# Optimization experiments

Measured on AMD Instinct MI355X. Metric: run time of the kernel, lower is better.

## Reference

```python
import jax, jax.numpy as jnp
import numpy as np

DN = ('NDHWC', 'DHWIO', 'NDHWC')
EPS = 1e-5  # torch BatchNorm default

def _conv(x, w, s):
    # Minkowski conv, kernel 3 centered: output coord j gathers input coords s*j + {-1,0,1}
    return jax.lax.conv_general_dilated(x, w, (s, s, s), ((1, 1),) * 3, dimension_numbers=DN)

def _convt(x, w):
    # stride-2 transpose conv, kernel 3 centered: output p gets input c where 2c in {p-1,p,p+1}
    return jax.lax.conv_general_dilated(x, w, (1, 1, 1), ((1, 2),) * 3,
                                        lhs_dilation=(2, 2, 2), dimension_numbers=DN)

def _down(m):
    # stride-2 coordinate map: a coarse voxel is active iff any of its 2x2x2 fine voxels is
    B, G = m.shape[0], m.shape[1]
    return m.reshape(B, G // 2, 2, G // 2, 2, G // 2, 2).any(axis=(2, 4, 6))

def _mbn(h, m, g, b):
    # MinkowskiBatchNorm: BatchNorm1d over the active (sparse) feature rows only
    mf = m[..., None].astype(h.dtype)
    h = h * mf
    cnt = jnp.maximum(jnp.sum(mf), 1.0)
    mean = jnp.sum(h, axis=(0, 1, 2, 3)) / cnt
    var = jnp.sum(((h - mean) * mf) ** 2, axis=(0, 1, 2, 3)) / cnt
    return ((h - mean) * jax.lax.rsqrt(var + EPS) * g + b) * mf


def setup_inputs() -> dict:
    key = jax.random.key(0)
    ks = jax.random.split(key, 8)
    B, G, Cin, Cout = 2, 64, 4, 16
    def w(k, shape, fan):
        return jax.random.normal(k, shape, jnp.float32) * np.float32(1.0 / np.sqrt(fan))
    return {
        'x': jax.random.normal(ks[0], (B, G, G, G, Cin), jnp.float32),
        'mask': jax.random.bernoulli(ks[1], 0.1, (B, G, G, G)),
        'w1': w(ks[2], (3, 3, 3, Cin, 8), 27 * Cin), 'g1': jnp.ones(8), 'b1': jnp.zeros(8),
        'w2': w(ks[3], (3, 3, 3, 8, 16), 27 * 8), 'g2': jnp.ones(16), 'b2': jnp.zeros(16),
        'w3': w(ks[4], (3, 3, 3, 16, 32), 27 * 16), 'g3': jnp.ones(32), 'b3': jnp.zeros(32),
        'w3t': w(ks[5], (3, 3, 3, 32, 16), 27 * 32), 'g3t': jnp.ones(16), 'b3t': jnp.zeros(16),
        'w2t': w(ks[6], (3, 3, 3, 32, 16), 27 * 32), 'g2t': jnp.ones(16), 'b2t': jnp.zeros(16),
        'w1x1': w(ks[7], (24, Cout), 24),
    }


def reference(x, mask, w1, g1, b1, w2, g2, b2, w3, g3, b3,
              w3t, g3t, b3t, w2t, g2t, b2t, w1x1):
    m1 = mask
    m2 = _down(m1)
    m4 = _down(m2)
    mf1 = m1[..., None].astype(x.dtype)

    xs = x * mf1                                      # sparse tensor: zero at inactive coords
    s1 = _mbn(_conv(xs, w1, 1), m1, g1, b1)           # block1, stride 1
    o = jax.nn.relu(s1)
    s2 = _mbn(_conv(o, w2, 2), m2, g2, b2)            # block2, stride 2
    o = jax.nn.relu(s2)
    s4 = _mbn(_conv(o, w3, 2), m4, g3, b3)            # block3, stride 4
    o = jax.nn.relu(s4)

    o = jax.nn.relu(_mbn(_convt(o, w3t), m2, g3t, b3t))   # block3_tr -> stride-2 coords
    o = jnp.concatenate([o, s2], axis=-1)                 # ME.cat(out, out_s2) -> 32 ch
    o = jax.nn.relu(_mbn(_convt(o, w2t), m1, g2t, b2t))   # block2_tr -> stride-1 coords
    o = jnp.concatenate([o, s1], axis=-1)                 # ME.cat(out, out_s1) -> 24 ch
    return jnp.einsum('bdhwc,co->bdhwo', o, w1x1) * mf1   # conv1_tr: 1x1x1 conv
```

## Files before the change

### kernel.cpp

```cpp
#include <hip/hip_runtime.h>

#define NVOX1 524288
#define NVOX2 65536
#define NVOX4 8192

#define ST_SUM1 16
#define ST_SQ1  24
#define ST_SUM2 32
#define ST_SQ2  48
#define ST_SUM3 64
#define ST_SQ3  96
#define ST_SUM3T 128
#define ST_SQ3T  144
#define ST_SUM2T 160
#define ST_SQ2T  176
#define FLAG_OFF 200
#define IC_N1 204
#define IC_N2 205
#define IC_N4 206
#define ST_ZERO 256

#define OFF_M1C 512
#define OFF_M2  (OFF_M1C + NVOX1)
#define OFF_M4  (OFF_M2 + NVOX2)
#define OFF_H1  (OFF_M4 + NVOX4)
#define OFF_S2  (OFF_H1 + NVOX1 * 8)
#define OFF_H3  (OFF_S2 + NVOX2 * 16)
#define OFF_T3  (OFF_H3 + NVOX4 * 32)
#define OFF_L1  (OFF_T3 + NVOX2 * 16)
#define OFF_L2  (OFF_L1 + NVOX1)
#define OFF_L4  (OFF_L2 + NVOX2)
#define OFF_BC1 (OFF_L4 + NVOX4)
#define OFF_BC2 (OFF_BC1 + 2048)
#define OFF_BC4 (OFF_BC2 + 256)

#define EPSBN 1e-5f

__device__ __forceinline__ void ttaps(int p, int gin, int* c, int* k, int* ok) {
  c[0] = p >> 1; k[0] = (p & 1) ? 0 : 1; ok[0] = 1;
  int cb = (p + 1) >> 1;
  int o = (p & 1) && (cb < gin);
  c[1] = o ? cb : 0; k[1] = 2; ok[1] = o;
}

__global__ __launch_bounds__(256) void k_detect(const unsigned int* __restrict__ m,
                                                int* __restrict__ flags) {
  int tid = blockIdx.x * 256 + threadIdx.x;
  int hasf = 0, hasb = 0;
  for (int i = tid; i < NVOX1; i += 256 * 256) {
    unsigned int v = m[i];
    if (v == 0x3F800000u) hasf = 1;
    else if (v > 1u) hasb = 1;
  }
  hasf = __syncthreads_or(hasf);
  hasb = __syncthreads_or(hasb);
  if (threadIdx.x == 0) {
    if (hasf) atomicOr(&flags[0], 1);
    if (hasb) atomicOr(&flags[1], 1);
  }
}

__global__ __launch_bounds__(256) void k_canon(const void* __restrict__ mraw,
                                               int* __restrict__ m1c,
                                               const int* __restrict__ flags,
                                               int* __restrict__ blkcnt1) {
  int idx = blockIdx.x * 256 + threadIdx.x;
  int isf = flags[0], isb = flags[1];
  int v;
  if (isf)      v = (((const float*)mraw)[idx] != 0.f);
  else if (isb) v = (((const unsigned char*)mraw)[idx] != 0);
  else          v = (((const int*)mraw)[idx] != 0);
  m1c[idx] = v;
  int c = __syncthreads_count(v);
  if (threadIdx.x == 0) blkcnt1[blockIdx.x] = c;
}

__global__ __launch_bounds__(256) void k_down1(const int* __restrict__ m1,
                                               int* __restrict__ m2,
                                               int* __restrict__ blkcnt2) {
  int idx = blockIdx.x * 256 + threadIdx.x;
  int x = idx & 31, y = (idx >> 5) & 31, z = (idx >> 10) & 31, b = idx >> 15;
  int any = 0;
#pragma unroll
  for (int dz = 0; dz < 2; dz++)
#pragma unroll
    for (int dy = 0; dy < 2; dy++)
#pragma unroll
      for (int dx = 0; dx < 2; dx++)
        any |= m1[((b * 64 + 2 * z + dz) * 64 + 2 * y + dy) * 64 + 2 * x + dx];
  any = any ? 1 : 0;
  m2[idx] = any;
  int c = __syncthreads_count(any);
  if (threadIdx.x == 0) blkcnt2[blockIdx.x] = c;
}

__global__ __launch_bounds__(256) void k_down2(const int* __restrict__ m2,
                                               int* __restrict__ m4,
                                               int* __restrict__ blkcnt4) {
  int idx = blockIdx.x * 256 + threadIdx.x;
  int x = idx & 15, y = (idx >> 4) & 15, z = (idx >> 8) & 15, b = idx >> 12;
  int any = 0;
#pragma unroll
  for (int dz = 0; dz < 2; dz++)
#pragma unroll
    for (int dy = 0; dy < 2; dy++)
#pragma unroll
      for (int dx = 0; dx < 2; dx++)
        any |= m2[((b * 32 + 2 * z + dz) * 32 + 2 * y + dy) * 32 + 2 * x + dx];
  any = any ? 1 : 0;
  m4[idx] = any;
  int c = __syncthreads_count(any);
  if (threadIdx.x == 0) blkcnt4[blockIdx.x] = c;
}

__global__ __launch_bounds__(1024) void k_scan(int* __restrict__ bc1,
                                               int* __restrict__ bc2,
                                               int* __restrict__ bc4,
                                               int* __restrict__ cnts) {
  __shared__ int sA[2048], sB[2048];
  int* a; int n; int outIdx;
  if (blockIdx.x == 0)      { a = bc1; n = 2048; outIdx = IC_N1; }
  else if (blockIdx.x == 1) { a = bc2; n = 256;  outIdx = IC_N2; }
  else                      { a = bc4; n = 32;   outIdx = IC_N4; }
  int t = threadIdx.x;
  int i0 = t, i1 = t + 1024;
  int v0 = (i0 < n) ? a[i0] : 0;
  int v1 = (i1 < n) ? a[i1] : 0;
  sA[i0] = v0; sA[i1] = v1;
  __syncthreads();
  int* src = sA; int* dst = sB;
  for (int st = 1; st < 2048; st <<= 1) {
    int x0 = src[i0]; if (i0 >= st) x0 += src[i0 - st];
    int x1 = src[i1]; if (i1 >= st) x1 += src[i1 - st];
    dst[i0] = x0; dst[i1] = x1;
    __syncthreads();
    int* tmp = src; src = dst; dst = tmp;
  }
  if (i0 < n) a[i0] = src[i0] - v0;
  if (i1 < n) a[i1] = src[i1] - v1;
  if (t == 0) cnts[outIdx] = src[2047];
}

__global__ __launch_bounds__(256) void k_scatter(const int* __restrict__ m1,
                                                 const int* __restrict__ m2,
                                                 const int* __restrict__ m4,
                                                 const int* __restrict__ bc1,
                                                 const int* __restrict__ bc2,
                                                 const int* __restrict__ bc4,
                                                 int* __restrict__ list1,
                                                 int* __restrict__ list2,
                                                 int* __restrict__ list4) {
  __shared__ int s_w[4];
  int bid = blockIdx.x, t = threadIdx.x;
  const int* mask; const int* base; int* list; int lb;
  if (bid < 2048)      { mask = m1; base = bc1; list = list1; lb = bid; }
  else if (bid < 2304) { mask = m2; base = bc2; list = list2; lb = bid - 2048; }
  else                 { mask = m4; base = bc4; list = list4; lb = bid - 2304; }
  int idx = lb * 256 + t;
  int act = mask[idx];
  unsigned long long b = __ballot(act != 0);
  int lane = t & 63, wid = t >> 6;
  if (lane == 0) s_w[wid] = __popcll(b);
  __syncthreads();
  int wbase = 0;
  for (int i = 0; i < wid; i++) wbase += s_w[i];
  if (act) {
    int pre = __popcll(b & ((1ull << lane) - 1ull));
    list[base[lb] + wbase + pre] = idx;
  }
}

__global__ __launch_bounds__(256) void k_conv1(const float* __restrict__ x,
                                               const int* __restrict__ m1,
                                               const int* __restrict__ list1,
                                               const int* __restrict__ cnts,
                                               const float* __restrict__ w,
                                               float* __restrict__ h1,
                                               float* __restrict__ stats) {
  __shared__ float s_w[27 * 32];
  __shared__ float s_sum[8], s_sq[8];
  int t = threadIdx.x;
  { const float4* w4 = (const float4*)w; float4* sw4 = (float4*)s_w;
    for (int i = t; i < 216; i += 256) sw4[i] = w4[i]; }
  if (t < 8) { s_sum[t] = 0.f; s_sq[t] = 0.f; }
  __syncthreads();
  int n = cnts[IC_N1];
  float sum[8], sq[8];
#pragma unroll
  for (int c = 0; c < 8; c++) { sum[c] = 0.f; sq[c] = 0.f; }
  for (int i = blockIdx.x * 256 + t; i < n; i += gridDim.x * 256) {
    int v = list1[i];
    int vx = v & 63, vy = (v >> 6) & 63, vz = (v >> 12) & 63, vb = v >> 18;
    float acc[8];
#pragma unroll
    for (int c = 0; c < 8; c++) acc[c] = 0.f;
#pragma unroll
    for (int kd = 0; kd < 3; kd++) { int d = vz + kd - 1; if ((unsigned)d >= 64u) continue;
#pragma unroll
      for (int kh = 0; kh < 3; kh++) { int h = vy + kh - 1; if ((unsigned)h >= 64u) continue;
#pragma unroll
        for (int kw = 0; kw < 3; kw++) { int ww = vx + kw - 1; if ((unsigned)ww >= 64u) continue;
          int ni = ((vb * 64 + d) * 64 + h) * 64 + ww;
          if (!m1[ni]) continue;
          float4 ip = *(const float4*)(x + (size_t)ni * 4);
          const float* wp = s_w + ((kd * 3 + kh) * 3 + kw) * 32;
#pragma unroll
          for (int co = 0; co < 8; co++) {
            float a = fmaf(ip.x, wp[co], acc[co]);
            a = fmaf(ip.y, wp[8 + co], a);
            a = fmaf(ip.z, wp[16 + co], a);
            acc[co] = fmaf(ip.w, wp[24 + co], a);
          }
        } } }
    float4* hp = (float4*)(h1 + (size_t)v * 8);
    float4 q0 = {acc[0], acc[1], acc[2], acc[3]};
    float4 q1 = {acc[4], acc[5], acc[6], acc[7]};
    hp[0] = q0; hp[1] = q1;
#pragma unroll
    for (int c = 0; c < 8; c++) { sum[c] += acc[c]; sq[c] += acc[c] * acc[c]; }
  }
#pragma unroll
  for (int off = 1; off < 64; off <<= 1)
#pragma unroll
    for (int c = 0; c < 8; c++) {
      sum[c] += __shfl_xor(sum[c], off, 64);
      sq[c]  += __shfl_xor(sq[c], off, 64);
    }
  if ((t & 63) == 0) {
#pragma unroll
    for (int c = 0; c < 8; c++) { atomicAdd(&s_sum[c], sum[c]); atomicAdd(&s_sq[c], sq[c]); }
  }
  __syncthreads();
  if (t < 8) {
    if (s_sum[t] != 0.f) atomicAdd(&stats[ST_SUM1 + t], s_sum[t]);
    if (s_sq[t]  != 0.f) atomicAdd(&stats[ST_SQ1 + t], s_sq[t]);
  }
}

__global__ __launch_bounds__(256) void k_conv2(const float* __restrict__ h1,
                                               const int* __restrict__ m1,
                                               const int* __restrict__ list2,
                                               const int* __restrict__ cnts,
                                               const float* __restrict__ w,
                                               const float* __restrict__ g1,
                                               const float* __restrict__ b1,
                                               float* __restrict__ s2,
                                               float* __restrict__ stats) {
  __shared__ float s_w[27 * 128];
  __shared__ float s_sc[8], s_bi[8];
  __shared__ float s_sum[16], s_sq[16];
  int t = threadIdx.x;
  { const float4* w4 = (const float4*)w; float4* sw4 = (float4*)s_w;
    for (int i = t; i < 864; i += 256) sw4[i] = w4[i]; }
  if (t < 8) {
    float cnt = fmaxf((float)cnts[IC_N1], 1.f);
    float mean = stats[ST_SUM1 + t] / cnt;
    float var = fmaxf(stats[ST_SQ1 + t] / cnt - mean * mean, 0.f);
    float sc = g1[t] * rsqrtf(var + EPSBN);
    s_sc[t] = sc; s_bi[t] = b1[t] - mean * sc;
  }
  if (t < 16) { s_sum[t] = 0.f; s_sq[t] = 0.f; }
  __syncthreads();
  int n = cnts[IC_N2];
  float sum[16], sq[16];
#pragma unroll
  for (int c = 0; c < 16; c++) { sum[c] = 0.f; sq[c] = 0.f; }
  for (int i = blockIdx.x * 256 + t; i < n; i += gridDim.x * 256) {
    int v = list2[i];
    int vx = v & 31, vy = (v >> 5) & 31, vz = (v >> 10) & 31, vb = v >> 15;
    float acc[16];
#pragma unroll
    for (int c = 0; c < 16; c++) acc[c] = 0.f;
#pragma unroll
    for (int kd = 0; kd < 3; kd++) { int d = 2 * vz + kd - 1; if (d < 0) continue;
#pragma unroll
      for (int kh = 0; kh < 3; kh++) { int h = 2 * vy + kh - 1; if (h < 0) continue;
#pragma unroll
        for (int kw = 0; kw < 3; kw++) { int ww = 2 * vx + kw - 1; if (ww < 0) continue;
          int ni = ((vb * 64 + d) * 64 + h) * 64 + ww;
          if (!m1[ni]) continue;
          float4 i0 = *(const float4*)(h1 + (size_t)ni * 8);
          float4 i1 = *(const float4*)(h1 + (size_t)ni * 8 + 4);
          float r[8] = {i0.x, i0.y, i0.z, i0.w, i1.x, i1.y, i1.z, i1.w};
          const float* wp = s_w + ((kd * 3 + kh) * 3 + kw) * 128;
#pragma unroll
          for (int ci = 0; ci < 8; ci++) {
            float vv = fmaxf(fmaf(r[ci], s_sc[ci], s_bi[ci]), 0.f);
#pragma unroll
            for (int co = 0; co < 16; co++) acc[co] = fmaf(vv, wp[ci * 16 + co], acc[co]);
          }
        } } }
    float4* sp = (float4*)(s2 + (size_t)v * 16);
#pragma unroll
    for (int cq = 0; cq < 4; cq++) {
      float4 q = {acc[cq * 4 + 0], acc[cq * 4 + 1], acc[cq * 4 + 2], acc[cq * 4 + 3]};
      sp[cq] = q;
    }
#pragma unroll
    for (int c = 0; c < 16; c++) { sum[c] += acc[c]; sq[c] += acc[c] * acc[c]; }
  }
#pragma unroll
  for (int off = 1; off < 64; off <<= 1)
#pragma unroll
    for (int c = 0; c < 16; c++) {
      sum[c] += __shfl_xor(sum[c], off, 64);
      sq[c]  += __shfl_xor(sq[c], off, 64);
    }
  if ((t & 63) == 0) {
#pragma unroll
    for (int c = 0; c < 16; c++) { atomicAdd(&s_sum[c], sum[c]); atomicAdd(&s_sq[c], sq[c]); }
  }
  __syncthreads();
  if (t < 16) {
    if (s_sum[t] != 0.f) atomicAdd(&stats[ST_SUM2 + t], s_sum[t]);
    if (s_sq[t]  != 0.f) atomicAdd(&stats[ST_SQ2 + t], s_sq[t]);
  }
}

__global__ __launch_bounds__(256) void k_conv3(const float* __restrict__ s2raw,
                                               const int* __restrict__ m2,
                                               const int* __restrict__ list4,
                                               const int* __restrict__ cnts,
                                               const float* __restrict__ w,
                                               const float* __restrict__ g2,
                                               const float* __restrict__ b2,
                                               float* __restrict__ h3,
                                               float* __restrict__ stats) {
  __shared__ float s_w[27 * 512];
  __shared__ float s_sc[16], s_bi[16];
  __shared__ float s_sum[32], s_sq[32];
  int t = threadIdx.x;
  { const float4* w4 = (const float4*)w; float4* sw4 = (float4*)s_w;
    for (int i = t; i < 3456; i += 256) sw4[i] = w4[i]; }
  if (t < 16) {
    float cnt = fmaxf((float)cnts[IC_N2], 1.f);
    float mean = stats[ST_SUM2 + t] / cnt;
    float var = fmaxf(stats[ST_SQ2 + t] / cnt - mean * mean, 0.f);
    float sc = g2[t] * rsqrtf(var + EPSBN);
    s_sc[t] = sc; s_bi[t] = b2[t] - mean * sc;
  }
  if (t < 32) { s_sum[t] = 0.f; s_sq[t] = 0.f; }
  __syncthreads();
  int cog = t & 3;
  int n = cnts[IC_N4] * 4;
  float sum[8], sq[8];
#pragma unroll
  for (int c = 0; c < 8; c++) { sum[c] = 0.f; sq[c] = 0.f; }
  for (int i = blockIdx.x * 256 + t; i < n; i += gridDim.x * 256) {
    int li = i >> 2;
    int v = list4[li];
    int vx = v & 15, vy = (v >> 4) & 15, vz = (v >> 8) & 15, vb = v >> 12;
    float acc[8];
#pragma unroll
    for (int c = 0; c < 8; c++) acc[c] = 0.f;
#pragma unroll
    for (int kd = 0; kd < 3; kd++) { int d = 2 * vz + kd - 1; if (d < 0) continue;
#pragma unroll
      for (int kh = 0; kh < 3; kh++) { int h = 2 * vy + kh - 1; if (h < 0) continue;
#pragma unroll
        for (int kw = 0; kw < 3; kw++) { int ww = 2 * vx + kw - 1; if (ww < 0) continue;
          int ni = ((vb * 32 + d) * 32 + h) * 32 + ww;
          if (!m2[ni]) continue;
          const float4* ip = (const float4*)(s2raw + (size_t)ni * 16);
          const float* wp = s_w + ((kd * 3 + kh) * 3 + kw) * 512 + cog * 8;
#pragma unroll
          for (int cq = 0; cq < 4; cq++) {
            float4 q = ip[cq];
            float rr[4] = {q.x, q.y, q.z, q.w};
#pragma unroll
            for (int j = 0; j < 4; j++) {
              int ci = cq * 4 + j;
              float vv = fmaxf(fmaf(rr[j], s_sc[ci], s_bi[ci]), 0.f);
#pragma unroll
              for (int co = 0; co < 8; co++) acc[co] = fmaf(vv, wp[ci * 32 + co], acc[co]);
            }
          }
        } } }
    float4* hp = (float4*)(h3 + (size_t)v * 32 + cog * 8);
    float4 q0 = {acc[0], acc[1], acc[2], acc[3]};
    float4 q1 = {acc[4], acc[5], acc[6], acc[7]};
    hp[0] = q0; hp[1] = q1;
#pragma unroll
    for (int c = 0; c < 8; c++) { sum[c] += acc[c]; sq[c] += acc[c] * acc[c]; }
  }
#pragma unroll
  for (int off = 4; off < 64; off <<= 1)
#pragma unroll
    for (int c = 0; c < 8; c++) {
      sum[c] += __shfl_xor(sum[c], off, 64);
      sq[c]  += __shfl_xor(sq[c], off, 64);
    }
  if ((t & 63) < 4) {
#pragma unroll
    for (int c = 0; c < 8; c++) {
      atomicAdd(&s_sum[cog * 8 + c], sum[c]);
      atomicAdd(&s_sq[cog * 8 + c], sq[c]);
    }
  }
  __syncthreads();
  if (t < 32) {
    if (s_sum[t] != 0.f) atomicAdd(&stats[ST_SUM3 + t], s_sum[t]);
    if (s_sq[t]  != 0.f) atomicAdd(&stats[ST_SQ3 + t], s_sq[t]);
  }
}

__global__ __launch_bounds__(256) void k_convt3(const float* __restrict__ h3raw,
                                                const int* __restrict__ m4,
                                                const int* __restrict__ list2,
                                                const int* __restrict__ cnts,
                                                const float* __restrict__ w,
                                                const float* __restrict__ g3,
                                                const float* __restrict__ b3,
                                                float* __restrict__ t3,
                                                float* __restrict__ stats) {
  __shared__ float s_w[27 * 512];
  __shared__ float s_sc[32], s_bi[32];
  __shared__ float s_sum[16], s_sq[16];
  int t = threadIdx.x;
  { const float4* w4 = (const float4*)w; float4* sw4 = (float4*)s_w;
    for (int i = t; i < 3456; i += 256) sw4[i] = w4[i]; }
  if (t < 32) {
    float cnt = fmaxf((float)cnts[IC_N4], 1.f);
    float mean = stats[ST_SUM3 + t] / cnt;
    float var = fmaxf(stats[ST_SQ3 + t] / cnt - mean * mean, 0.f);
    float sc = g3[t] * rsqrtf(var + EPSBN);
    s_sc[t] = sc; s_bi[t] = b3[t] - mean * sc;
  }
  if (t < 16) { s_sum[t] = 0.f; s_sq[t] = 0.f; }
  __syncthreads();
  int cog = t & 1;
  int n = cnts[IC_N2] * 2;
  float sum[8], sq[8];
#pragma unroll
  for (int c = 0; c < 8; c++) { sum[c] = 0.f; sq[c] = 0.f; }
  for (int i = blockIdx.x * 256 + t; i < n; i += gridDim.x * 256) {
    int li = i >> 1;
    int v = list2[li];
    int px = v & 31, py = (v >> 5) & 31, pz = (v >> 10) & 31, vb = v >> 15;
    int czv[2], kzv[2], okz[2], cyv[2], kyv[2], oky[2], cxv[2], kxv[2], okx[2];
    ttaps(pz, 16, czv, kzv, okz);
    ttaps(py, 16, cyv, kyv, oky);
    ttaps(px, 16, cxv, kxv, okx);
    float acc[8];
#pragma unroll
    for (int c = 0; c < 8; c++) acc[c] = 0.f;
#pragma unroll
    for (int dz = 0; dz < 2; dz++)
#pragma unroll
      for (int dy = 0; dy < 2; dy++)
#pragma unroll
        for (int dx = 0; dx < 2; dx++) {
          if (!(okz[dz] & oky[dy] & okx[dx])) continue;
          int ni = ((vb * 16 + czv[dz]) * 16 + cyv[dy]) * 16 + cxv[dx];
          if (!m4[ni]) continue;
          const float4* ip = (const float4*)(h3raw + (size_t)ni * 32);
          const float* wp = s_w + ((kzv[dz] * 3 + kyv[dy]) * 3 + kxv[dx]) * 512 + cog * 8;
#pragma unroll
          for (int cq = 0; cq < 8; cq++) {
            float4 q = ip[cq];
            float rr[4] = {q.x, q.y, q.z, q.w};
#pragma unroll
            for (int j = 0; j < 4; j++) {
              int ci = cq * 4 + j;
              float vv = fmaxf(fmaf(rr[j], s_sc[ci], s_bi[ci]), 0.f);
#pragma unroll
              for (int co = 0; co < 8; co++) acc[co] = fmaf(vv, wp[ci * 16 + co], acc[co]);
            }
          }
        }
    float4* op = (float4*)(t3 + (size_t)v * 16 + cog * 8);
    float4 q0 = {acc[0], acc[1], acc[2], acc[3]};
    float4 q1 = {acc[4], acc[5], acc[6], acc[7]};
    op[0] = q0; op[1] = q1;
#pragma unroll
    for (int c = 0; c < 8; c++) { sum[c] += acc[c]; sq[c] += acc[c] * acc[c]; }
  }
#pragma unroll
  for (int off = 2; off < 64; off <<= 1)
#pragma unroll
    for (int c = 0; c < 8; c++) {
      sum[c] += __shfl_xor(sum[c], off, 64);
      sq[c]  += __shfl_xor(sq[c], off, 64);
    }
  if ((t & 63) < 2) {
#pragma unroll
    for (int c = 0; c < 8; c++) {
      atomicAdd(&s_sum[cog * 8 + c], sum[c]);
      atomicAdd(&s_sq[cog * 8 + c], sq[c]);
    }
  }
  __syncthreads();
  if (t < 16) {
    if (s_sum[t] != 0.f) atomicAdd(&stats[ST_SUM3T + t], s_sum[t]);
    if (s_sq[t]  != 0.f) atomicAdd(&stats[ST_SQ3T + t], s_sq[t]);
  }
}

__global__ __launch_bounds__(256) void k_convt2(const float* __restrict__ t3raw,
                                                const float* __restrict__ s2raw,
                                                const int* __restrict__ m2,
                                                const int* __restrict__ list1,
                                                const int* __restrict__ cnts,
                                                const float* __restrict__ w,
                                                const float* __restrict__ g3t,
                                                const float* __restrict__ b3t,
                                                const float* __restrict__ g2,
                                                const float* __restrict__ b2,
                                                float* __restrict__ outraw,
                                                float* __restrict__ stats) {
  __shared__ float s_w[27 * 512];
  __shared__ float s_sct[16], s_bit[16], s_sc2[16], s_bi2[16];
  __shared__ float s_sum[16], s_sq[16];
  int t = threadIdx.x;
  { const float4* w4 = (const float4*)w; float4* sw4 = (float4*)s_w;
    for (int i = t; i < 3456; i += 256) sw4[i] = w4[i]; }
  if (t < 16) {
    float cnt = fmaxf((float)cnts[IC_N2], 1.f);
    float mean = stats[ST_SUM3T + t] / cnt;
    float var = fmaxf(stats[ST_SQ3T + t] / cnt - mean * mean, 0.f);
    float sc = g3t[t] * rsqrtf(var + EPSBN);
    s_sct[t] = sc; s_bit[t] = b3t[t] - mean * sc;
    float mean2 = stats[ST_SUM2 + t] / cnt;
    float var2 = fmaxf(stats[ST_SQ2 + t] / cnt - mean2 * mean2, 0.f);
    float sc2 = g2[t] * rsqrtf(var2 + EPSBN);
    s_sc2[t] = sc2; s_bi2[t] = b2[t] - mean2 * sc2;
    s_sum[t] = 0.f; s_sq[t] = 0.f;
  }
  __syncthreads();
  int cog = t & 1;
  int n = cnts[IC_N1] * 2;
  float sum[8], sq[8];
#pragma unroll
  for (int c = 0; c < 8; c++) { sum[c] = 0.f; sq[c] = 0.f; }
  for (int i = blockIdx.x * 256 + t; i < n; i += gridDim.x * 256) {
    int li = i >> 1;
    int v = list1[li];
    int px = v & 63, py = (v >> 6) & 63, pz = (v >> 12) & 63, vb = v >> 18;
    int czv[2], kzv[2], okz[2], cyv[2], kyv[2], oky[2], cxv[2], kxv[2], okx[2];
    ttaps(pz, 32, czv, kzv, okz);
    ttaps(py, 32, cyv, kyv, oky);
    ttaps(px, 32, cxv, kxv, okx);
    float acc[8];
#pragma unroll
    for (int c = 0; c < 8; c++) acc[c] = 0.f;
#pragma unroll
    for (int dz = 0; dz < 2; dz++)
#pragma unroll
      for (int dy = 0; dy < 2; dy++)
#pragma unroll
        for (int dx = 0; dx < 2; dx++) {
          if (!(okz[dz] & oky[dy] & okx[dx])) continue;
          int ni = ((vb * 32 + czv[dz]) * 32 + cyv[dy]) * 32 + cxv[dx];
          if (!m2[ni]) continue;
          const float4* tp = (const float4*)(t3raw + (size_t)ni * 16);
          const float4* sp = (const float4*)(s2raw + (size_t)ni * 16);
          const float* wp = s_w + ((kzv[dz] * 3 + kyv[dy]) * 3 + kxv[dx]) * 512 + cog * 8;
#pragma unroll
          for (int cq = 0; cq < 4; cq++) {
            float4 q = tp[cq];
            float rr[4] = {q.x, q.y, q.z, q.w};
#pragma unroll
            for (int j = 0; j < 4; j++) {
              int ci = cq * 4 + j;
              float vv = fmaxf(fmaf(rr[j], s_sct[ci], s_bit[ci]), 0.f);
#pragma unroll
              for (int co = 0; co < 8; co++) acc[co] = fmaf(vv, wp[ci * 16 + co], acc[co]);
            }
          }
#pragma unroll
          for (int cq = 0; cq < 4; cq++) {
            float4 q = sp[cq];
            float rr[4] = {q.x, q.y, q.z, q.w};
#pragma unroll
            for (int j = 0; j < 4; j++) {
              int ci = cq * 4 + j;
              float vv = fmaf(rr[j], s_sc2[ci], s_bi2[ci]);
#pragma unroll
              for (int co = 0; co < 8; co++) acc[co] = fmaf(vv, wp[(16 + ci) * 16 + co], acc[co]);
            }
          }
        }
    float4* op = (float4*)(outraw + (size_t)v * 16 + cog * 8);
    float4 q0 = {acc[0], acc[1], acc[2], acc[3]};
    float4 q1 = {acc[4], acc[5], acc[6], acc[7]};
    op[0] = q0; op[1] = q1;
#pragma unroll
    for (int c = 0; c < 8; c++) { sum[c] += acc[c]; sq[c] += acc[c] * acc[c]; }
  }
#pragma unroll
  for (int off = 2; off < 64; off <<= 1)
#pragma unroll
    for (int c = 0; c < 8; c++) {
      sum[c] += __shfl_xor(sum[c], off, 64);
      sq[c]  += __shfl_xor(sq[c], off, 64);
    }
  if ((t & 63) < 2) {
#pragma unroll
    for (int c = 0; c < 8; c++) {
      atomicAdd(&s_sum[cog * 8 + c], sum[c]);
      atomicAdd(&s_sq[cog * 8 + c], sq[c]);
    }
  }
  __syncthreads();
  if (t < 16) {
    if (s_sum[t] != 0.f) atomicAdd(&stats[ST_SUM2T + t], s_sum[t]);
    if (s_sq[t]  != 0.f) atomicAdd(&stats[ST_SQ2T + t], s_sq[t]);
  }
}

__global__ __launch_bounds__(256) void k_final(float* __restrict__ out,
                                               const float* __restrict__ h1raw,
                                               const int* __restrict__ list1,
                                               const int* __restrict__ cnts,
                                               const float* __restrict__ g2t,
                                               const float* __restrict__ b2t,
                                               const float* __restrict__ g1,
                                               const float* __restrict__ b1,
                                               const float* __restrict__ w1x1,
                                               const float* __restrict__ stats) {
  __shared__ float s_sc[16], s_bi[16], s_sc1[8], s_bi1[8], s_w[384];
  int t = threadIdx.x;
  for (int i = t; i < 384; i += 256) s_w[i] = w1x1[i];
  if (t < 16) {
    float cnt = fmaxf((float)cnts[IC_N1], 1.f);
    float mean = stats[ST_SUM2T + t] / cnt;
    float var = fmaxf(stats[ST_SQ2T + t] / cnt - mean * mean, 0.f);
    float sc = g2t[t] * rsqrtf(var + EPSBN);
    s_sc[t] = sc; s_bi[t] = b2t[t] - mean * sc;
  }
  if (t < 8) {
    float cnt = fmaxf((float)cnts[IC_N1], 1.f);
    float mean = stats[ST_SUM1 + t] / cnt;
    float var = fmaxf(stats[ST_SQ1 + t] / cnt - mean * mean, 0.f);
    float sc = g1[t] * rsqrtf(var + EPSBN);
    s_sc1[t] = sc; s_bi1[t] = b1[t] - mean * sc;
  }
  __syncthreads();
  int n = cnts[IC_N1];
  for (int i = blockIdx.x * 256 + t; i < n; i += gridDim.x * 256) {
    int v = list1[i];
    float* op = out + (size_t)v * 16;
    float t2[16];
    {
      const float4* op4 = (const float4*)op;
#pragma unroll
      for (int cq = 0; cq < 4; cq++) {
        float4 q = op4[cq];
        t2[cq * 4 + 0] = fmaxf(fmaf(q.x, s_sc[cq * 4 + 0], s_bi[cq * 4 + 0]), 0.f);
        t2[cq * 4 + 1] = fmaxf(fmaf(q.y, s_sc[cq * 4 + 1], s_bi[cq * 4 + 1]), 0.f);
        t2[cq * 4 + 2] = fmaxf(fmaf(q.z, s_sc[cq * 4 + 2], s_bi[cq * 4 + 2]), 0.f);
        t2[cq * 4 + 3] = fmaxf(fmaf(q.w, s_sc[cq * 4 + 3], s_bi[cq * 4 + 3]), 0.f);
      }
    }
    float s1v[8];
    {
      const float4* sp4 = (const float4*)(h1raw + (size_t)v * 8);
#pragma unroll
      for (int cq = 0; cq < 2; cq++) {
        float4 q = sp4[cq];
        s1v[cq * 4 + 0] = fmaf(q.x, s_sc1[cq * 4 + 0], s_bi1[cq * 4 + 0]);
        s1v[cq * 4 + 1] = fmaf(q.y, s_sc1[cq * 4 + 1], s_bi1[cq * 4 + 1]);
        s1v[cq * 4 + 2] = fmaf(q.z, s_sc1[cq * 4 + 2], s_bi1[cq * 4 + 2]);
        s1v[cq * 4 + 3] = fmaf(q.w, s_sc1[cq * 4 + 3], s_bi1[cq * 4 + 3]);
      }
    }
    float o[16];
#pragma unroll
    for (int oc = 0; oc < 16; oc++) o[oc] = 0.f;
#pragma unroll
    for (int c = 0; c < 16; c++) {
      float vv = t2[c];
#pragma unroll
      for (int oc = 0; oc < 16; oc++) o[oc] = fmaf(vv, s_w[c * 16 + oc], o[oc]);
    }
#pragma unroll
    for (int c = 0; c < 8; c++) {
      float vv = s1v[c];
#pragma unroll
      for (int oc = 0; oc < 16; oc++) o[oc] = fmaf(vv, s_w[(16 + c) * 16 + oc], o[oc]);
    }
    float4* op4 = (float4*)op;
#pragma unroll
    for (int cq = 0; cq < 4; cq++) {
      float4 q = {o[cq * 4 + 0], o[cq * 4 + 1], o[cq * 4 + 2], o[cq * 4 + 3]};
      op4[cq] = q;
    }
  }
}

extern "C" void kernel_launch(void* const* d_in, const int* in_sizes, int n_in,
                              void* d_out, int out_size, void* d_ws, size_t ws_size,
                              hipStream_t stream) {
  const float* x    = (const float*)d_in[0];
  const void*  mraw = d_in[1];
  const float* w1   = (const float*)d_in[2];
  const float* g1   = (const float*)d_in[3];
  const float* b1   = (const float*)d_in[4];
  const float* w2   = (const float*)d_in[5];
  const float* g2   = (const float*)d_in[6];
  const float* b2   = (const float*)d_in[7];
  const float* w3   = (const float*)d_in[8];
  const float* g3   = (const float*)d_in[9];
  const float* b3   = (const float*)d_in[10];
  const float* w3t  = (const float*)d_in[11];
  const float* g3t  = (const float*)d_in[12];
  const float* b3t  = (const float*)d_in[13];
  const float* w2t  = (const float*)d_in[14];
  const float* g2t  = (const float*)d_in[15];
  const float* b2t  = (const float*)d_in[16];
  const float* w1x1 = (const float*)d_in[17];

  float* ws = (float*)d_ws;
  float* stats = ws;
  int* cnts = (int*)ws;
  int* flags = (int*)(ws + FLAG_OFF);
  int* m1c = (int*)(ws + OFF_M1C);
  int* m2  = (int*)(ws + OFF_M2);
  int* m4  = (int*)(ws + OFF_M4);
  float* h1 = ws + OFF_H1;
  float* s2 = ws + OFF_S2;
  float* h3 = ws + OFF_H3;
  float* t3 = ws + OFF_T3;
  int* list1 = (int*)(ws + OFF_L1);
  int* list2 = (int*)(ws + OFF_L2);
  int* list4 = (int*)(ws + OFF_L4);
  int* bc1 = (int*)(ws + OFF_BC1);
  int* bc2 = (int*)(ws + OFF_BC2);
  int* bc4 = (int*)(ws + OFF_BC4);
  float* out = (float*)d_out;

  hipMemsetAsync(ws, 0, ST_ZERO * sizeof(float), stream);
  hipMemsetAsync(d_out, 0, (size_t)out_size * sizeof(float), stream);
  k_detect<<<256, 256, 0, stream>>>((const unsigned int*)mraw, flags);
  k_canon<<<NVOX1 / 256, 256, 0, stream>>>(mraw, m1c, flags, bc1);
  k_down1<<<NVOX2 / 256, 256, 0, stream>>>(m1c, m2, bc2);
  k_down2<<<NVOX4 / 256, 256, 0, stream>>>(m2, m4, bc4);
  k_scan<<<3, 1024, 0, stream>>>(bc1, bc2, bc4, cnts);
  k_scatter<<<2048 + 256 + 32, 256, 0, stream>>>(m1c, m2, m4, bc1, bc2, bc4, list1, list2, list4);
  k_conv1<<<256, 256, 0, stream>>>(x, m1c, list1, cnts, w1, h1, stats);
  k_conv2<<<256, 256, 0, stream>>>(h1, m1c, list2, cnts, w2, g1, b1, s2, stats);
  k_conv3<<<512, 256, 0, stream>>>(s2, m2, list4, cnts, w3, g2, b2, h3, stats);
  k_convt3<<<512, 256, 0, stream>>>(h3, m4, list2, cnts, w3t, g3, b3, t3, stats);
  k_convt2<<<512, 256, 0, stream>>>(t3, s2, m2, list1, cnts, w2t, g3t, b3t, g2, b2, out, stats);
  k_final<<<256, 256, 0, stream>>>(out, h1, list1, cnts, g2t, b2t, g1, b1, w1x1, stats);
}
```

Before: 192.8 us.

## Split output channels across blockIdx.y and stage only per-group weights in LDS

```diff
diff --git a/kernel.cpp b/kernel.cpp
--- a/kernel.cpp
+++ b/kernel.cpp
@@ -41,6 +41,20 @@
   int cb = (p + 1) >> 1;
   int o = (p & 1) && (cb < gin);
   c[1] = o ? cb : 0; k[1] = 2; ok[1] = o;
+}
+
+__device__ __forceinline__ void stat_flush8(float* sum, float* sq, float* s_sum, float* s_sq, int t) {
+#pragma unroll
+  for (int off = 1; off < 64; off <<= 1)
+#pragma unroll
+    for (int c = 0; c < 8; c++) {
+      sum[c] += __shfl_xor(sum[c], off, 64);
+      sq[c]  += __shfl_xor(sq[c], off, 64);
+    }
+  if ((t & 63) == 0) {
+#pragma unroll
+    for (int c = 0; c < 8; c++) { atomicAdd(&s_sum[c], sum[c]); atomicAdd(&s_sq[c], sq[c]); }
+  }
 }
 
 __global__ __launch_bounds__(256) void k_detect(const unsigned int* __restrict__ m,
@@ -219,17 +233,7 @@
 #pragma unroll
     for (int c = 0; c < 8; c++) { sum[c] += acc[c]; sq[c] += acc[c] * acc[c]; }
   }
-#pragma unroll
-  for (int off = 1; off < 64; off <<= 1)
-#pragma unroll
-    for (int c = 0; c < 8; c++) {
-      sum[c] += __shfl_xor(sum[c], off, 64);
-      sq[c]  += __shfl_xor(sq[c], off, 64);
-    }
-  if ((t & 63) == 0) {
-#pragma unroll
-    for (int c = 0; c < 8; c++) { atomicAdd(&s_sum[c], sum[c]); atomicAdd(&s_sq[c], sq[c]); }
-  }
+  stat_flush8(sum, sq, s_sum, s_sq, t);
   __syncthreads();
   if (t < 8) {
     if (s_sum[t] != 0.f) atomicAdd(&stats[ST_SUM1 + t], s_sum[t]);
@@ -246,31 +250,33 @@
                                                const float* __restrict__ b1,
                                                float* __restrict__ s2,
                                                float* __restrict__ stats) {
-  __shared__ float s_w[27 * 128];
+  __shared__ float s_w[27 * 8 * 8];
   __shared__ float s_sc[8], s_bi[8];
-  __shared__ float s_sum[16], s_sq[16];
-  int t = threadIdx.x;
-  { const float4* w4 = (const float4*)w; float4* sw4 = (float4*)s_w;
-    for (int i = t; i < 864; i += 256) sw4[i] = w4[i]; }
+  __shared__ float s_sum[8], s_sq[8];
+  int t = threadIdx.x, g = blockIdx.y;
+  for (int i = t; i < 432; i += 256) {
+    int r = i >> 1, half = i & 1;
+    *(float4*)(s_w + r * 8 + half * 4) = *(const float4*)(w + r * 16 + g * 8 + half * 4);
+  }
   if (t < 8) {
     float cnt = fmaxf((float)cnts[IC_N1], 1.f);
     float mean = stats[ST_SUM1 + t] / cnt;
     float var = fmaxf(stats[ST_SQ1 + t] / cnt - mean * mean, 0.f);
     float sc = g1[t] * rsqrtf(var + EPSBN);
     s_sc[t] = sc; s_bi[t] = b1[t] - mean * sc;
-  }
-  if (t < 16) { s_sum[t] = 0.f; s_sq[t] = 0.f; }
+    s_sum[t] = 0.f; s_sq[t] = 0.f;
+  }
   __syncthreads();
   int n = cnts[IC_N2];
-  float sum[16], sq[16];
-#pragma unroll
-  for (int c = 0; c < 16; c++) { sum[c] = 0.f; sq[c] = 0.f; }
+  float sum[8], sq[8];
+#pragma unroll
+  for (int c = 0; c < 8; c++) { sum[c] = 0.f; sq[c] = 0.f; }
   for (int i = blockIdx.x * 256 + t; i < n; i += gridDim.x * 256) {
     int v = list2[i];
     int vx = v & 31, vy = (v >> 5) & 31, vz = (v >> 10) & 31, vb = v >> 15;
-    float acc[16];
-#pragma unroll
-    for (int c = 0; c < 16; c++) acc[c] = 0.f;
+    float acc[8];
+#pragma unroll
+    for (int c = 0; c < 8; c++) acc[c] = 0.f;
 #pragma unroll
     for (int kd = 0; kd < 3; kd++) { int d = 2 * vz + kd - 1; if (d < 0) continue;
 #pragma unroll
@@ -282,38 +288,26 @@
           float4 i0 = *(const float4*)(h1 + (size_t)ni * 8);
           float4 i1 = *(const float4*)(h1 + (size_t)ni * 8 + 4);
           float r[8] = {i0.x, i0.y, i0.z, i0.w, i1.x, i1.y, i1.z, i1.w};
-          const float* wp = s_w + ((kd * 3 + kh) * 3 + kw) * 128;
+          const float* wp = s_w + ((kd * 3 + kh) * 3 + kw) * 64;
 #pragma unroll
           for (int ci = 0; ci < 8; ci++) {
             float vv = fmaxf(fmaf(r[ci], s_sc[ci], s_bi[ci]), 0.f);
 #pragma unroll
-            for (int co = 0; co < 16; co++) acc[co] = fmaf(vv, wp[ci * 16 + co], acc[co]);
+            for (int co = 0; co < 8; co++) acc[co] = fmaf(vv, wp[ci * 8 + co], acc[co]);
           }
         } } }
-    float4* sp = (float4*)(s2 + (size_t)v * 16);
-#pragma unroll
-    for (int cq = 0; cq < 4; cq++) {
-      float4 q = {acc[cq * 4 + 0], acc[cq * 4 + 1], acc[cq * 4 + 2], acc[cq * 4 + 3]};
-      sp[cq] = q;
-    }
-#pragma unroll
-    for (int c = 0; c < 16; c++) { sum[c] += acc[c]; sq[c] += acc[c] * acc[c]; }
-  }
-#pragma unroll
-  for (int off = 1; off < 64; off <<= 1)
-#pragma unroll
-    for (int c = 0; c < 16; c++) {
-      sum[c] += __shfl_xor(sum[c], off, 64);
-      sq[c]  += __shfl_xor(sq[c], off, 64);
-    }
-  if ((t & 63) == 0) {
-#pragma unroll
-    for (int c = 0; c < 16; c++) { atomicAdd(&s_sum[c], sum[c]); atomicAdd(&s_sq[c], sq[c]); }
-  }
-  __syncthreads();
-  if (t < 16) {
-    if (s_sum[t] != 0.f) atomicAdd(&stats[ST_SUM2 + t], s_sum[t]);
-    if (s_sq[t]  != 0.f) atomicAdd(&stats[ST_SQ2 + t], s_sq[t]);
+    float4* sp = (float4*)(s2 + (size_t)v * 16 + g * 8);
+    float4 q0 = {acc[0], acc[1], acc[2], acc[3]};
+    float4 q1 = {acc[4], acc[5], acc[6], acc[7]};
+    sp[0] = q0; sp[1] = q1;
+#pragma unroll
+    for (int c = 0; c < 8; c++) { sum[c] += acc[c]; sq[c] += acc[c] * acc[c]; }
+  }
+  stat_flush8(sum, sq, s_sum, s_sq, t);
+  __syncthreads();
+  if (t < 8) {
+    if (s_sum[t] != 0.f) atomicAdd(&stats[ST_SUM2 + g * 8 + t], s_sum[t]);
+    if (s_sq[t]  != 0.f) atomicAdd(&stats[ST_SQ2 + g * 8 + t], s_sq[t]);
   }
 }
 
@@ -326,12 +320,14 @@
                                                const float* __restrict__ b2,
                                                float* __restrict__ h3,
                                                float* __restrict__ stats) {
-  __shared__ float s_w[27 * 512];
+  __shared__ float s_w[27 * 16 * 8];
   __shared__ float s_sc[16], s_bi[16];
-  __shared__ float s_sum[32], s_sq[32];
-  int t = threadIdx.x;
-  { const float4* w4 = (const float4*)w; float4* sw4 = (float4*)s_w;
-    for (int i = t; i < 3456; i += 256) sw4[i] = w4[i]; }
+  __shared__ float s_sum[8], s_sq[8];
+  int t = threadIdx.x, g = blockIdx.y;
+  for (int i = t; i < 864; i += 256) {
+    int r = i >> 1, half = i & 1;
+    *(float4*)(s_w + r * 8 + half * 4) = *(const float4*)(w + r * 32 + g * 8 + half * 4);
+  }
   if (t < 16) {
     float cnt = fmaxf((float)cnts[IC_N2], 1.f);
     float mean = stats[ST_SUM2 + t] / cnt;
@@ -339,16 +335,14 @@
     float sc = g2[t] * rsqrtf(var + EPSBN);
     s_sc[t] = sc; s_bi[t] = b2[t] - mean * sc;
   }
-  if (t < 32) { s_sum[t] = 0.f; s_sq[t] = 0.f; }
-  __syncthreads();
-  int cog = t & 3;
-  int n = cnts[IC_N4] * 4;
+  if (t < 8) { s_sum[t] = 0.f; s_sq[t] = 0.f; }
+  __syncthreads();
+  int n = cnts[IC_N4];
   float sum[8], sq[8];
 #pragma unroll
   for (int c = 0; c < 8; c++) { sum[c] = 0.f; sq[c] = 0.f; }
   for (int i = blockIdx.x * 256 + t; i < n; i += gridDim.x * 256) {
-    int li = i >> 2;
-    int v = list4[li];
+    int v = list4[i];
     int vx = v & 15, vy = (v >> 4) & 15, vz = (v >> 8) & 15, vb = v >> 12;
     float acc[8];
 #pragma unroll
@@ -362,7 +356,7 @@
           int ni = ((vb * 32 + d) * 32 + h) * 32 + ww;
           if (!m2[ni]) continue;
           const float4* ip = (const float4*)(s2raw + (size_t)ni * 16);
-          const float* wp = s_w + ((kd * 3 + kh) * 3 + kw) * 512 + cog * 8;
+          const float* wp = s_w + ((kd * 3 + kh) * 3 + kw) * 128;
 #pragma unroll
           for (int cq = 0; cq < 4; cq++) {
             float4 q = ip[cq];
@@ -372,35 +366,22 @@
               int ci = cq * 4 + j;
               float vv = fmaxf(fmaf(rr[j], s_sc[ci], s_bi[ci]), 0.f);
 #pragma unroll
-              for (int co = 0; co < 8; co++) acc[co] = fmaf(vv, wp[ci * 32 + co], acc[co]);
+              for (int co = 0; co < 8; co++) acc[co] = fmaf(vv, wp[ci * 8 + co], acc[co]);
             }
           }
         } } }
-    float4* hp = (float4*)(h3 + (size_t)v * 32 + cog * 8);
+    float4* hp = (float4*)(h3 + (size_t)v * 32 + g * 8);
     float4 q0 = {acc[0], acc[1], acc[2], acc[3]};
     float4 q1 = {acc[4], acc[5], acc[6], acc[7]};
     hp[0] = q0; hp[1] = q1;
 #pragma unroll
     for (int c = 0; c < 8; c++) { sum[c] += acc[c]; sq[c] += acc[c] * acc[c]; }
   }
-#pragma unroll
-  for (int off = 4; off < 64; off <<= 1)
-#pragma unroll
-    for (int c = 0; c < 8; c++) {
-      sum[c] += __shfl_xor(sum[c], off, 64);
-      sq[c]  += __shfl_xor(sq[c], off, 64);
-    }
-  if ((t & 63) < 4) {
-#pragma unroll
-    for (int c = 0; c < 8; c++) {
-      atomicAdd(&s_sum[cog * 8 + c], sum[c]);
-      atomicAdd(&s_sq[cog * 8 + c], sq[c]);
-    }
-  }
-  __syncthreads();
-  if (t < 32) {
-    if (s_sum[t] != 0.f) atomicAdd(&stats[ST_SUM3 + t], s_sum[t]);
-    if (s_sq[t]  != 0.f) atomicAdd(&stats[ST_SQ3 + t], s_sq[t]);
+  stat_flush8(sum, sq, s_sum, s_sq, t);
+  __syncthreads();
+  if (t < 8) {
+    if (s_sum[t] != 0.f) atomicAdd(&stats[ST_SUM3 + g * 8 + t], s_sum[t]);
+    if (s_sq[t]  != 0.f) atomicAdd(&stats[ST_SQ3 + g * 8 + t], s_sq[t]);
   }
 }
 
@@ -413,12 +394,14 @@
                                                 const float* __restrict__ b3,
                                                 float* __restrict__ t3,
                                                 float* __restrict__ stats) {
-  __shared__ float s_w[27 * 512];
+  __shared__ float s_w[27 * 32 * 8];
   __shared__ float s_sc[32], s_bi[32];
-  __shared__ float s_sum[16], s_sq[16];
-  int t = threadIdx.x;
-  { const float4* w4 = (const float4*)w; float4* sw4 = (float4*)s_w;
-    for (int i = t; i < 3456; i += 256) sw4[i] = w4[i]; }
+  __shared__ float s_sum[8], s_sq[8];
+  int t = threadIdx.x, g = blockIdx.y;
+  for (int i = t; i < 1728; i += 256) {
+    int r = i >> 1, half = i & 1;
+    *(float4*)(s_w + r * 8 + half * 4) = *(const float4*)(w + r * 16 + g * 8 + half * 4);
+  }
   if (t < 32) {
     float cnt = fmaxf((float)cnts[IC_N4], 1.f);
     float mean = stats[ST_SUM3 + t] / cnt;
@@ -426,16 +409,14 @@
     float sc = g3[t] * rsqrtf(var + EPSBN);
     s_sc[t] = sc; s_bi[t] = b3[t] - mean * sc;
   }
-  if (t < 16) { s_sum[t] = 0.f; s_sq[t] = 0.f; }
-  __syncthreads();
-  int cog = t & 1;
-  int n = cnts[IC_N2] * 2;
+  if (t < 8) { s_sum[t] = 0.f; s_sq[t] = 0.f; }
+  __syncthreads();
+  int n = cnts[IC_N2];
   float sum[8], sq[8];
 #pragma unroll
   for (int c = 0; c < 8; c++) { sum[c] = 0.f; sq[c] = 0.f; }
   for (int i = blockIdx.x * 256 + t; i < n; i += gridDim.x * 256) {
-    int li = i >> 1;
-    int v = list2[li];
+    int v = list2[i];
     int px = v & 31, py = (v >> 5) & 31, pz = (v >> 10) & 31, vb = v >> 15;
     int czv[2], kzv[2], okz[2], cyv[2], kyv[2], oky[2], cxv[2], kxv[2], okx[2];
     ttaps(pz, 16, czv, kzv, okz);
@@ -454,7 +435,7 @@
           int ni = ((vb * 16 + czv[dz]) * 16 + cyv[dy]) * 16 + cxv[dx];
           if (!m4[ni]) continue;
           const float4* ip = (const float4*)(h3raw + (size_t)ni * 32);
-          const float* wp = s_w + ((kzv[dz] * 3 + kyv[dy]) * 3 + kxv[dx]) * 512 + cog * 8;
+          const float* wp = s_w + ((kzv[dz] * 3 + kyv[dy]) * 3 + kxv[dx]) * 256;
 #pragma unroll
           for (int cq = 0; cq < 8; cq++) {
             float4 q = ip[cq];
@@ -464,35 +445,22 @@
               int ci = cq * 4 + j;
               float vv = fmaxf(fmaf(rr[j], s_sc[ci], s_bi[ci]), 0.f);
 #pragma unroll
-              for (int co = 0; co < 8; co++) acc[co] = fmaf(vv, wp[ci * 16 + co], acc[co]);
+              for (int co = 0; co < 8; co++) acc[co] = fmaf(vv, wp[ci * 8 + co], acc[co]);
             }
           }
         }
-    float4* op = (float4*)(t3 + (size_t)v * 16 + cog * 8);
+    float4* op = (float4*)(t3 + (size_t)v * 16 + g * 8);
     float4 q0 = {acc[0], acc[1], acc[2], acc[3]};
     float4 q1 = {acc[4], acc[5], acc[6], acc[7]};
     op[0] = q0; op[1] = q1;
 #pragma unroll
     for (int c = 0; c < 8; c++) { sum[c] += acc[c]; sq[c] += acc[c] * acc[c]; }
   }
-#pragma unroll
-  for (int off = 2; off < 64; off <<= 1)
-#pragma unroll
-    for (int c = 0; c < 8; c++) {
-      sum[c] += __shfl_xor(sum[c], off, 64);
-      sq[c]  += __shfl_xor(sq[c], off, 64);
-    }
-  if ((t & 63) < 2) {
-#pragma unroll
-    for (int c = 0; c < 8; c++) {
-      atomicAdd(&s_sum[cog * 8 + c], sum[c]);
-      atomicAdd(&s_sq[cog * 8 + c], sq[c]);
-    }
-  }
-  __syncthreads();
-  if (t < 16) {
-    if (s_sum[t] != 0.f) atomicAdd(&stats[ST_SUM3T + t], s_sum[t]);
-    if (s_sq[t]  != 0.f) atomicAdd(&stats[ST_SQ3T + t], s_sq[t]);
+  stat_flush8(sum, sq, s_sum, s_sq, t);
+  __syncthreads();
+  if (t < 8) {
+    if (s_sum[t] != 0.f) atomicAdd(&stats[ST_SUM3T + g * 8 + t], s_sum[t]);
+    if (s_sq[t]  != 0.f) atomicAdd(&stats[ST_SQ3T + g * 8 + t], s_sq[t]);
   }
 }
 
@@ -508,12 +476,14 @@
                                                 const float* __restrict__ b2,
                                                 float* __restrict__ outraw,
                                                 float* __restrict__ stats) {
-  __shared__ float s_w[27 * 512];
+  __shared__ float s_w[27 * 32 * 8];
   __shared__ float s_sct[16], s_bit[16], s_sc2[16], s_bi2[16];
-  __shared__ float s_sum[16], s_sq[16];
-  int t = threadIdx.x;
-  { const float4* w4 = (const float4*)w; float4* sw4 = (float4*)s_w;
-    for (int i = t; i < 3456; i += 256) sw4[i] = w4[i]; }
+  __shared__ float s_sum[8], s_sq[8];
+  int t = threadIdx.x, g = blockIdx.y;
+  for (int i = t; i < 1728; i += 256) {
+    int r = i >> 1, half = i & 1;
+    *(float4*)(s_w + r * 8 + half * 4) = *(const float4*)(w + r * 16 + g * 8 + half * 4);
+  }
   if (t < 16) {
     float cnt = fmaxf((float)cnts[IC_N2], 1.f);
     float mean = stats[ST_SUM3T + t] / cnt;
@@ -524,17 +494,15 @@
     float var2 = fmaxf(stats[ST_SQ2 + t] / cnt - mean2 * mean2, 0.f);
     float sc2 = g2[t] * rsqrtf(var2 + EPSBN);
     s_sc2[t] = sc2; s_bi2[t] = b2[t] - mean2 * sc2;
-    s_sum[t] = 0.f; s_sq[t] = 0.f;
-  }
-  __syncthreads();
-  int cog = t & 1;
-  int n = cnts[IC_N1] * 2;
+  }
+  if (t < 8) { s_sum[t] = 0.f; s_sq[t] = 0.f; }
+  __syncthreads();
+  int n = cnts[IC_N1];
   float sum[8], sq[8];
 #pragma unroll
   for (int c = 0; c < 8; c++) { sum[c] = 0.f; sq[c] = 0.f; }
   for (int i = blockIdx.x * 256 + t; i < n; i += gridDim.x * 256) {
-    int li = i >> 1;
-    int v = list1[li];
+    int v = list1[i];
     int px = v & 63, py = (v >> 6) & 63, pz = (v >> 12) & 63, vb = v >> 18;
     int czv[2], kzv[2], okz[2], cyv[2], kyv[2], oky[2], cxv[2], kxv[2], okx[2];
     ttaps(pz, 32, czv, kzv, okz);
@@ -554,7 +522,7 @@
           if (!m2[ni]) continue;
           const float4* tp = (const float4*)(t3raw + (size_t)ni * 16);
           const float4* sp = (const float4*)(s2raw + (size_t)ni * 16);
-          const float* wp = s_w + ((kzv[dz] * 3 + kyv[dy]) * 3 + kxv[dx]) * 512 + cog * 8;
+          const float* wp = s_w + ((kzv[dz] * 3 + kyv[dy]) * 3 + kxv[dx]) * 256;
 #pragma unroll
           for (int cq = 0; cq < 4; cq++) {
             float4 q = tp[cq];
@@ -564,7 +532,7 @@
               int ci = cq * 4 + j;
               float vv = fmaxf(fmaf(rr[j], s_sct[ci], s_bit[ci]), 0.f);
 #pragma unroll
-              for (int co = 0; co < 8; co++) acc[co] = fmaf(vv, wp[ci * 16 + co], acc[co]);
+              for (int co = 0; co < 8; co++) acc[co] = fmaf(vv, wp[ci * 8 + co], acc[co]);
             }
           }
 #pragma unroll
@@ -576,35 +544,22 @@
               int ci = cq * 4 + j;
               float vv = fmaf(rr[j], s_sc2[ci], s_bi2[ci]);
 #pragma unroll
-              for (int co = 0; co < 8; co++) acc[co] = fmaf(vv, wp[(16 + ci) * 16 + co], acc[co]);
+              for (int co = 0; co < 8; co++) acc[co] = fmaf(vv, wp[(16 + ci) * 8 + co], acc[co]);
             }
           }
         }
-    float4* op = (float4*)(outraw + (size_t)v * 16 + cog * 8);
+    float4* op = (float4*)(outraw + (size_t)v * 16 + g * 8);
     float4 q0 = {acc[0], acc[1], acc[2], acc[3]};
     float4 q1 = {acc[4], acc[5], acc[6], acc[7]};
     op[0] = q0; op[1] = q1;
 #pragma unroll
     for (int c = 0; c < 8; c++) { sum[c] += acc[c]; sq[c] += acc[c] * acc[c]; }
   }
-#pragma unroll
-  for (int off = 2; off < 64; off <<= 1)
-#pragma unroll
-    for (int c = 0; c < 8; c++) {
-      sum[c] += __shfl_xor(sum[c], off, 64);
-      sq[c]  += __shfl_xor(sq[c], off, 64);
-    }
-  if ((t & 63) < 2) {
-#pragma unroll
-    for (int c = 0; c < 8; c++) {
-      atomicAdd(&s_sum[cog * 8 + c], sum[c]);
-      atomicAdd(&s_sq[cog * 8 + c], sq[c]);
-    }
-  }
-  __syncthreads();
-  if (t < 16) {
-    if (s_sum[t] != 0.f) atomicAdd(&stats[ST_SUM2T + t], s_sum[t]);
-    if (s_sq[t]  != 0.f) atomicAdd(&stats[ST_SQ2T + t], s_sq[t]);
+  stat_flush8(sum, sq, s_sum, s_sq, t);
+  __syncthreads();
+  if (t < 8) {
+    if (s_sum[t] != 0.f) atomicAdd(&stats[ST_SUM2T + g * 8 + t], s_sum[t]);
+    if (s_sq[t]  != 0.f) atomicAdd(&stats[ST_SQ2T + g * 8 + t], s_sq[t]);
   }
 }
 
@@ -738,9 +693,9 @@
   k_scan<<<3, 1024, 0, stream>>>(bc1, bc2, bc4, cnts);
   k_scatter<<<2048 + 256 + 32, 256, 0, stream>>>(m1c, m2, m4, bc1, bc2, bc4, list1, list2, list4);
   k_conv1<<<256, 256, 0, stream>>>(x, m1c, list1, cnts, w1, h1, stats);
-  k_conv2<<<256, 256, 0, stream>>>(h1, m1c, list2, cnts, w2, g1, b1, s2, stats);
-  k_conv3<<<512, 256, 0, stream>>>(s2, m2, list4, cnts, w3, g2, b2, h3, stats);
-  k_convt3<<<512, 256, 0, stream>>>(h3, m4, list2, cnts, w3t, g3, b3, t3, stats);
-  k_convt2<<<512, 256, 0, stream>>>(t3, s2, m2, list1, cnts, w2t, g3t, b3t, g2, b2, out, stats);
+  k_conv2<<<dim3(256, 2), 256, 0, stream>>>(h1, m1c, list2, cnts, w2, g1, b1, s2, stats);
+  k_conv3<<<dim3(32, 4), 256, 0, stream>>>(s2, m2, list4, cnts, w3, g2, b2, h3, stats);
+  k_convt3<<<dim3(256, 2), 256, 0, stream>>>(h3, m4, list2, cnts, w3t, g3, b3, t3, stats);
+  k_convt2<<<dim3(256, 2), 256, 0, stream>>>(t3, s2, m2, list1, cnts, w2t, g3t, b3t, g2, b2, out, stats);
   k_final<<<256, 256, 0, stream>>>(out, h1, list1, cnts, g2t, b2t, g1, b1, w1x1, stats);
 }
```

Measured after the change: 197.3 us. 2.3% more time.
